# Kernel optimization log

Measured on AMD Instinct MI355X. Metric: run time of the kernel, lower is better.

## Reference

```python
import jax, jax.numpy as jnp
import numpy as np

N, E, P = 50000, 800000, 100000
IN, HID, H, L = 128, 128, 8, 3
D = HID // H


def setup_inputs() -> dict:
    key = jax.random.key(0)
    ks = jax.random.split(key, 24)
    rn = lambda k, shape, s: (jax.random.normal(k, shape, jnp.float32) * s)
    inp = {
        'x': jax.random.normal(ks[0], (N, IN), jnp.float32),
        'edge_src': jax.random.randint(ks[1], (E,), 0, N, jnp.int32),
        'edge_dst': jax.random.randint(ks[2], (E,), 0, N, jnp.int32),
        'edge_w': jax.random.uniform(ks[3], (E,), jnp.float32),
        'pos_src': jax.random.randint(ks[4], (P,), 0, N, jnp.int32),
        'pos_dst': jax.random.randint(ks[5], (P,), 0, N, jnp.int32),
        'neg_src': jax.random.randint(ks[6], (P,), 0, N, jnp.int32),
        'neg_dst': jax.random.randint(ks[7], (P,), 0, N, jnp.int32),
        # input projection
        'W_in': rn(ks[8], (IN, HID), IN ** -0.5),
        'b_in': jnp.zeros((HID,), jnp.float32),
        # per-layer HGT params (single ntype/etype -> plain matrices)
        'Wk': rn(ks[9], (L, HID, HID), HID ** -0.5),
        'Wq': rn(ks[10], (L, HID, HID), HID ** -0.5),
        'Wv': rn(ks[11], (L, HID, HID), HID ** -0.5),
        'att_w': rn(ks[12], (L, H, D, D), D ** -0.5),
        'msg_w': rn(ks[13], (L, H, D, D), D ** -0.5),
        'pri': jnp.ones((L, H), jnp.float32),
        'Wa': rn(ks[14], (L, HID, HID), HID ** -0.5),
        'skip': jnp.ones((L,), jnp.float32),
        # predictor MLP
        'W1': rn(ks[15], (HID, HID // 2), HID ** -0.5),
        'b1': jnp.zeros((HID // 2,), jnp.float32),
        'W2': rn(ks[16], (HID // 2, HID // 4), (HID // 2) ** -0.5),
        'b2': jnp.zeros((HID // 4,), jnp.float32),
        'W3': rn(ks[17], (HID // 4, 1), (HID // 4) ** -0.5),
        'b3': jnp.zeros((1,), jnp.float32),
    }
    return inp


def _hgt_forward(x, edge_src, edge_dst, edge_w, pos_src, pos_dst, neg_src, neg_dst,
                 W_in, b_in, Wk, Wq, Wv, att_w, msg_w, pri, Wa, skip,
                 W1, b1, W2, b2, W3, b3):
    n = x.shape[0]
    nheads = att_w.shape[1]
    d = att_w.shape[2]
    sqrt_d = jnp.asarray(d ** 0.5, x.dtype)
    h = jax.nn.relu(x @ W_in + b_in)
    nlayers = Wk.shape[0]
    for l in range(nlayers):
        k = (h @ Wk[l]).reshape(n, nheads, d)
        q = (h @ Wq[l]).reshape(n, nheads, d)
        v = (h @ Wv[l]).reshape(n, nheads, d)
        # relation-specific per-head transforms (etype constant -> node-level)
        kw = jnp.einsum('nhd,hde->nhe', k, att_w[l])
        mv = jnp.einsum('nhd,hde->nhe', v, msg_w[l])
        # per-edge attention logits [E, H]
        a = (kw[edge_src] * q[edge_dst]).sum(-1) * pri[l] / sqrt_d
        # edge softmax grouped by destination node
        amax = jax.ops.segment_max(a, edge_dst, num_segments=n)[edge_dst]
        ex = jnp.exp(a - amax)
        denom = jax.ops.segment_sum(ex, edge_dst, num_segments=n)[edge_dst]
        attn = ex / denom
        # weighted messages + scatter-sum  [E,H,D] -> [N,H,D]
        m = mv[edge_src] * edge_w[:, None, None] * attn[:, :, None]
        agg = jax.ops.segment_sum(m, edge_dst, num_segments=n).reshape(n, nheads * d)
        hn = agg @ Wa[l]  # linear_a (dropout is identity in eval)
        alpha = jax.nn.sigmoid(skip[l])
        h = hn * alpha + h * (1.0 - alpha)
        if l != nlayers - 1:
            h = jax.nn.relu(h)  # inter-layer relu (dropout identity)
    def predictor(z):
        z = jax.nn.leaky_relu(z @ W1 + b1, 0.2)
        z = jax.nn.leaky_relu(z @ W2 + b2, 0.2)
        return z @ W3 + b3
    h_pos = predictor(h[pos_src] * h[pos_dst])
    h_neg = predictor(h[neg_src] * h[neg_dst])
    return h_pos, h_neg, h


def reference(x, edge_src, edge_dst, edge_w, pos_src, pos_dst, neg_src, neg_dst,
              W_in, b_in, Wk, Wq, Wv, att_w, msg_w, pri, Wa, skip,
              W1, b1, W2, b2, W3, b3):
    return _hgt_forward(x, edge_src, edge_dst, edge_w, pos_src, pos_dst,
                        neg_src, neg_dst, W_in, b_in, Wk, Wq, Wv, att_w,
                        msg_w, pri, Wa, skip, W1, b1, W2, b2, W3, b3)
```

## Files before the change

kernel.cpp:

```cpp
#include <hip/hip_runtime.h>
#include <cstddef>

#define N_NODES 50000
#define N_EDGES 800000
#define N_PAIRS 100000

typedef float floatx4 __attribute__((ext_vector_type(4)));
typedef _Float16 half2v __attribute__((ext_vector_type(2)));
typedef _Float16 half4v __attribute__((ext_vector_type(4)));
typedef _Float16 half8v __attribute__((ext_vector_type(8)));

__device__ inline size_t packA(int m, int k, int K) {
  return ((size_t)((m >> 4) * (K >> 5) + (k >> 5)) << 9) +
         ((((unsigned)k >> 3) & 3) << 7) + ((m & 15) << 3) + (k & 7);
}

__device__ inline float fold_val(int l, int r, int j, const float* Wk, const float* Wq,
                                 const float* Wv, const float* att, const float* msg,
                                 const float* pri) {
  if (j >= 128 && j < 256) return Wq[(l * 128 + r) * 128 + (j - 128)];
  int jj = j & 127, hh = jj >> 4, e = jj & 15;
  const float* W = (j < 128) ? Wk : Wv;
  const float* T = (j < 128) ? att : msg;
  float s = 0.f;
#pragma unroll
  for (int d = 0; d < 16; d++)
    s += W[(l * 128 + r) * 128 + hh * 16 + d] * T[((l * 8 + hh) * 16 + d) * 16 + e];
  if (j < 128) s *= pri[l * 8 + hh] * 0.25f;
  return s;
}

__global__ void wprep_kernel(const float* __restrict__ W_in, const float* __restrict__ Wk,
                             const float* __restrict__ Wq, const float* __restrict__ Wv,
                             const float* __restrict__ att, const float* __restrict__ msg,
                             const float* __restrict__ pri, const float* __restrict__ Wa,
                             const float* __restrict__ W1, const float* __restrict__ W2,
                             _Float16* Wint, _Float16* Wcat, _Float16* Waf,
                             _Float16* W1f, _Float16* W2f) {
  int gid = blockIdx.x * 256 + threadIdx.x;
  float v;
  _Float16* dt;
  size_t o;
  if (gid < 16384) {
    int n = gid >> 7, k = gid & 127;
    v = W_in[k * 128 + n];
    dt = Wint; o = packA(n, k, 128);
  } else if (gid < 163840) {
    int t = gid - 16384;
    int l = t / 49152, u = t - l * 49152;
    int n = u >> 7, k = u & 127;
    v = fold_val(l, k, n, Wk, Wq, Wv, att, msg, pri);
    dt = Wcat + (size_t)l * 49152;
    o = packA(n, k, 128);
  } else if (gid < 212992) {
    int t = gid - 163840;
    int l = t / 16384, u = t & 16383;
    int n = u >> 7, k = u & 127;
    v = Wa[(size_t)l * 16384 + k * 128 + n];
    dt = Waf + (size_t)l * 16384;
    o = packA(n, k, 128);
  } else if (gid < 221184) {
    int u = gid - 212992;
    int n = u >> 7, k = u & 127;
    v = W1[k * 64 + n];
    dt = W1f; o = packA(n, k, 128);
  } else if (gid < 225280) {
    int u = gid - 221184;
    int n = u >> 6, k = u & 63;
    v = (n < 32) ? W2[k * 32 + n] : 0.f;
    dt = W2f; o = packA(n, k, 64);
  } else {
    return;
  }
  dt[o] = (_Float16)v;
}

__global__ void hist_kernel(const int* __restrict__ dst, int* __restrict__ deg, int E) {
  int g = blockIdx.x * blockDim.x + threadIdx.x;
  if (g < E) atomicAdd(&deg[dst[g]], 1);
}

__global__ void scanA_kernel(const int* __restrict__ deg, int* __restrict__ offs,
                             int* __restrict__ bsum, int n) {
  __shared__ int sm[256];
  int t = threadIdx.x;
  int i = blockIdx.x * 256 + t;
  int v = (i < n) ? ((deg[i] + 15) & ~15) : 0;
  sm[t] = v;
  __syncthreads();
  for (int off = 1; off < 256; off <<= 1) {
    int u = (t >= off) ? sm[t - off] : 0;
    __syncthreads();
    sm[t] += u;
    __syncthreads();
  }
  if (i < n) offs[i] = sm[t] - v;
  if (t == 255) bsum[blockIdx.x] = sm[255];
}

__global__ void scanB_kernel(const int* __restrict__ bsum, int* __restrict__ boff,
                             int* __restrict__ offs, int nb, int n) {
  __shared__ int sm[256];
  int t = threadIdx.x;
  int v = (t < nb) ? bsum[t] : 0;
  sm[t] = v;
  __syncthreads();
  for (int off = 1; off < 256; off <<= 1) {
    int u = (t >= off) ? sm[t - off] : 0;
    __syncthreads();
    sm[t] += u;
    __syncthreads();
  }
  boff[t] = sm[t] - v;
  if (t == nb - 1) offs[n] = sm[t];
}

__global__ void scanC_kernel(int* __restrict__ offs, const int* __restrict__ boff,
                             int* __restrict__ cursor, int n) {
  int i = blockIdx.x * 256 + threadIdx.x;
  if (i < n) {
    int o = offs[i] + boff[blockIdx.x];
    offs[i] = o;
    cursor[i] = o;
  }
}

__global__ void scatter_kernel(const int* __restrict__ src, const int* __restrict__ dst,
                               const float* __restrict__ w, int* __restrict__ cursor,
                               int2* __restrict__ eld, int E) {
  int g = blockIdx.x * blockDim.x + threadIdx.x;
  if (g < E) {
    int d = dst[g];
    int p = atomicAdd(&cursor[d], 1);
    eld[p] = make_int2(src[g], __float_as_int(w[g]));
  }
}

__global__ void bhist_kernel(const int* __restrict__ deg, int* __restrict__ bh, int n) {
  __shared__ int lh[256];
  int t = threadIdx.x;
  lh[t] = 0;
  __syncthreads();
  int i = blockIdx.x * 256 + t;
  if (i < n) atomicAdd(&lh[min(deg[i], 255)], 1);
  __syncthreads();
  if (lh[t]) atomicAdd(&bh[t], lh[t]);
}
__global__ void bscan_kernel(const int* __restrict__ bh, int* __restrict__ bcur) {
  __shared__ int sm[256];
  int t = threadIdx.x;
  int v = bh[255 - t];
  sm[t] = v;
  __syncthreads();
  for (int off = 1; off < 256; off <<= 1) {
    int u = (t >= off) ? sm[t - off] : 0;
    __syncthreads();
    sm[t] += u;
    __syncthreads();
  }
  bcur[255 - t] = sm[t] - v;
}
__global__ void bscatter_kernel(const int* __restrict__ deg, int* __restrict__ bcur,
                                int* __restrict__ perm, int n) {
  __shared__ int lh[256], lbase[256];
  int t = threadIdx.x;
  lh[t] = 0;
  __syncthreads();
  int i = blockIdx.x * 256 + t;
  int b = 0, local = 0;
  if (i < n) {
    b = min(deg[i], 255);
    local = atomicAdd(&lh[b], 1);
  }
  __syncthreads();
  int cnt = lh[t];
  lbase[t] = cnt ? atomicAdd(&bcur[t], cnt) : 0;
  __syncthreads();
  if (i < n) perm[lbase[b] + local] = i;
}

template <int FIRST>
__global__ __launch_bounds__(256) void fused_layer(
    const float* __restrict__ x, const _Float16* __restrict__ aggp,
    const _Float16* __restrict__ Wg1, const float* __restrict__ bias,
    const float* __restrict__ skipv, _Float16* __restrict__ hbuf,
    const _Float16* __restrict__ Wcat_l,
    _Float16* __restrict__ kwmv, _Float16* __restrict__ qbuf, int M) {
  int tid = threadIdx.x;
  int wave = tid >> 6, lane = tid & 63;
  int l16 = lane & 15, q = lane >> 4;
  int g = q, mloc = l16;
  int tile = blockIdx.x * 4 + wave;
  int m0 = tile * 16;
  bool alive = m0 < M;
  int tileC = alive ? tile : 0;

  __shared__ _Float16 htile_s[4][2048];
  __shared__ float ldsT_s[4][16 * 68];
  _Float16* htile = htile_s[wave];
  float* myT = ldsT_s[wave];

  half8v a[4];
#pragma unroll
  for (int kc = 0; kc < 4; kc++) {
    if (FIRST) {
      int row = min(m0 + l16, M - 1);
      const float* p = x + (size_t)row * 128 + kc * 32 + q * 8;
      float4 u0 = *(const float4*)p, u1 = *(const float4*)(p + 4);
      float f[8] = {u0.x, u0.y, u0.z, u0.w, u1.x, u1.y, u1.z, u1.w};
      half8v hv;
#pragma unroll
      for (int i = 0; i < 8; i++) hv[i] = (_Float16)f[i];
      a[kc] = hv;
    } else {
      a[kc] = *(const half8v*)(aggp + (size_t)tileC * 2048 + (kc << 9) + lane * 8);
    }
  }

  float alpha = 1.f, beta = 0.f;
  if (!FIRST) {
    float sv = *skipv;
    alpha = 1.f / (1.f + __expf(-sv));
    beta = 1.f - alpha;
  }

  floatx4 acc1[8];
#pragma unroll
  for (int nt = 0; nt < 8; nt++) acc1[nt] = (floatx4){0.f, 0.f, 0.f, 0.f};
#pragma unroll
  for (int kc = 0; kc < 4; kc++) {
    half8v b[8];
#pragma unroll
    for (int nt = 0; nt < 8; nt++)
      b[nt] = *(const half8v*)(Wg1 + (size_t)nt * 2048 + (kc << 9) + lane * 8);
#pragma unroll
    for (int nt = 0; nt < 8; nt++)
      acc1[nt] = __builtin_amdgcn_mfma_f32_16x16x32_f16(a[kc], b[nt], acc1[nt], 0, 0, 0);
  }

#pragma unroll
  for (int p = 0; p < 2; p++) {
    __syncthreads();
#pragma unroll
    for (int ntl = 0; ntl < 4; ntl++)
#pragma unroll
      for (int r = 0; r < 4; r++)
        myT[(q * 4 + r) * 68 + ntl * 16 + l16] = acc1[p * 4 + ntl][r];
    __syncthreads();
#pragma unroll
    for (int kc2 = 0; kc2 < 2; kc2++) {
      const float* rp = myT + mloc * 68 + kc2 * 32 + g * 8;
      floatx4 v0 = *(const floatx4*)rp;
      floatx4 v1 = *(const floatx4*)(rp + 4);
      float vals[8] = {v0[0], v0[1], v0[2], v0[3], v1[0], v1[1], v1[2], v1[3]};
      int col0 = p * 64 + kc2 * 32 + g * 8;
      size_t pbaseL = ((size_t)(tileC * 4 + (col0 >> 5)) << 9) + (size_t)lane * 8;
      if (FIRST) {
        float4 bb0 = *(const float4*)&bias[col0];
        float4 bb1 = *(const float4*)&bias[col0 + 4];
        float bbv[8] = {bb0.x, bb0.y, bb0.z, bb0.w, bb1.x, bb1.y, bb1.z, bb1.w};
#pragma unroll
        for (int j = 0; j < 8; j++) vals[j] = fmaxf(vals[j] + bbv[j], 0.f);
      } else {
        half8v hv = *(const half8v*)(hbuf + pbaseL);
#pragma unroll
        for (int j = 0; j < 8; j++)
          vals[j] = fmaxf(alpha * vals[j] + beta * (float)hv[j], 0.f);
      }
      half8v h8;
#pragma unroll
      for (int j = 0; j < 8; j++) h8[j] = (_Float16)vals[j];
      *(half8v*)(htile + (((p * 2 + kc2) << 9) + (g << 7) + (mloc << 3))) = h8;
      if (alive) *(half8v*)(hbuf + pbaseL) = h8;
    }
  }

  for (int c = 0; c < 6; c++) {
    floatx4 acc2[4];
#pragma unroll
    for (int nt = 0; nt < 4; nt++) acc2[nt] = (floatx4){0.f, 0.f, 0.f, 0.f};
#pragma unroll
    for (int kc = 0; kc < 4; kc++) {
      half8v af = *(const half8v*)(htile + ((kc << 9) + lane * 8));
      half8v b[4];
#pragma unroll
      for (int nt = 0; nt < 4; nt++)
        b[nt] = *(const half8v*)(Wcat_l + (size_t)(c * 4 + nt) * 2048 + (kc << 9) + lane * 8);
#pragma unroll
      for (int nt = 0; nt < 4; nt++)
        acc2[nt] = __builtin_amdgcn_mfma_f32_16x16x32_f16(af, b[nt], acc2[nt], 0, 0, 0);
    }
    __syncthreads();
#pragma unroll
    for (int ntl = 0; ntl < 4; ntl++)
#pragma unroll
      for (int r = 0; r < 4; r++)
        myT[(q * 4 + r) * 68 + ntl * 16 + l16] = acc2[ntl][r];
    __syncthreads();
    if (alive) {
      int row = m0 + mloc;
#pragma unroll
      for (int kc2 = 0; kc2 < 2; kc2++) {
        const float* rp = myT + mloc * 68 + kc2 * 32 + g * 8;
        floatx4 v0 = *(const floatx4*)rp;
        floatx4 v1 = *(const floatx4*)(rp + 4);
        int col0 = c * 64 + kc2 * 32 + g * 8;
        int region = col0 >> 7;
        if (region == 1) {
          half8v h8;
#pragma unroll
          for (int j = 0; j < 4; j++) {
            h8[j] = (_Float16)v0[j];
            h8[j + 4] = (_Float16)v1[j];
          }
          *(half8v*)&qbuf[(size_t)row * 128 + (col0 - 128)] = h8;
        } else {
          int cc = col0 & 127;
          size_t base = (size_t)row * 256 + (size_t)(cc >> 2) * 8 + (region == 2 ? 4 : 0);
          half4v h0, h1;
#pragma unroll
          for (int j = 0; j < 4; j++) {
            h0[j] = (_Float16)v0[j];
            h1[j] = (_Float16)v1[j];
          }
          *(half4v*)&kwmv[base] = h0;
          *(half4v*)&kwmv[base + 8] = h1;
        }
      }
    }
  }
}

__global__ __launch_bounds__(256) void gemm_last(
    const _Float16* __restrict__ aggp, const _Float16* __restrict__ Wg1,
    const float* __restrict__ skipv, const _Float16* __restrict__ hbuf,
    float* __restrict__ hfinal, _Float16* __restrict__ hrow, int M) {
  int tid = threadIdx.x;
  int wave = tid >> 6, lane = tid & 63;
  int l16 = lane & 15, q = lane >> 4;
  int g = q, mloc = l16;
  int tile = blockIdx.x * 4 + wave;
  int m0 = tile * 16;
  bool alive = m0 < M;
  int tileC = alive ? tile : 0;

  __shared__ float ldsT_s[4][16 * 68];
  float* myT = ldsT_s[wave];

  half8v a[4];
#pragma unroll
  for (int kc = 0; kc < 4; kc++)
    a[kc] = *(const half8v*)(aggp + (size_t)tileC * 2048 + (kc << 9) + lane * 8);

  float sv = *skipv;
  float alpha = 1.f / (1.f + __expf(-sv));
  float beta = 1.f - alpha;

  floatx4 acc1[8];
#pragma unroll
  for (int nt = 0; nt < 8; nt++) acc1[nt] = (floatx4){0.f, 0.f, 0.f, 0.f};
#pragma unroll
  for (int kc = 0; kc < 4; kc++) {
    half8v b[8];
#pragma unroll
    for (int nt = 0; nt < 8; nt++)
      b[nt] = *(const half8v*)(Wg1 + (size_t)nt * 2048 + (kc << 9) + lane * 8);
#pragma unroll
    for (int nt = 0; nt < 8; nt++)
      acc1[nt] = __builtin_amdgcn_mfma_f32_16x16x32_f16(a[kc], b[nt], acc1[nt], 0, 0, 0);
  }

#pragma unroll
  for (int p = 0; p < 2; p++) {
    __syncthreads();
#pragma unroll
    for (int ntl = 0; ntl < 4; ntl++)
#pragma unroll
      for (int r = 0; r < 4; r++)
        myT[(q * 4 + r) * 68 + ntl * 16 + l16] = acc1[p * 4 + ntl][r];
    __syncthreads();
    if (alive) {
      int row = m0 + mloc;
#pragma unroll
      for (int kc2 = 0; kc2 < 2; kc2++) {
        const float* rp = myT + mloc * 68 + kc2 * 32 + g * 8;
        floatx4 v0 = *(const floatx4*)rp;
        floatx4 v1 = *(const floatx4*)(rp + 4);
        float vals[8] = {v0[0], v0[1], v0[2], v0[3], v1[0], v1[1], v1[2], v1[3]};
        int col0 = p * 64 + kc2 * 32 + g * 8;
        size_t pbase = ((size_t)(tile * 4 + (col0 >> 5)) << 9) + (size_t)lane * 8;
        half8v hv = *(const half8v*)(hbuf + pbase);
#pragma unroll
        for (int j = 0; j < 8; j++) vals[j] = alpha * vals[j] + beta * (float)hv[j];
        *(float4*)&hfinal[(size_t)row * 128 + col0] =
            make_float4(vals[0], vals[1], vals[2], vals[3]);
        *(float4*)&hfinal[(size_t)row * 128 + col0 + 4] =
            make_float4(vals[4], vals[5], vals[6], vals[7]);
        half8v h8;
#pragma unroll
        for (int j = 0; j < 8; j++) h8[j] = (_Float16)vals[j];
        *(half8v*)&hrow[(size_t)row * 128 + col0] = h8;
      }
    }
  }
}

__global__ __launch_bounds__(256) void pred_fused(
    const _Float16* __restrict__ hrow,
    const int* __restrict__ ps, const int* __restrict__ pd,
    const int* __restrict__ ns, const int* __restrict__ nd,
    const _Float16* __restrict__ W1f, const float* __restrict__ b1,
    const _Float16* __restrict__ W2f, const float* __restrict__ b2,
    const float* __restrict__ W3, const float* __restrict__ b3,
    float* __restrict__ outd, int M) {
  int tid = threadIdx.x;
  int wave = tid >> 6, lane = tid & 63;
  int l16 = lane & 15, q = lane >> 4;
  int g = q, mloc = l16;
  int tile = blockIdx.x * 4 + wave;
  int m0 = tile * 16;
  bool alive = m0 < M;

  __shared__ _Float16 t1_s[4][1024];
  __shared__ float ldsT_s[4][16 * 68];
  _Float16* t1tile = t1_s[wave];
  float* myT = ldsT_s[wave];

  int gr = min(m0 + l16, M - 1);
  bool pos = gr < N_PAIRS;
  int idx = pos ? gr : gr - N_PAIRS;
  int pa = pos ? ps[idx] : ns[idx];
  int pb = pos ? pd[idx] : nd[idx];

  half8v a[4];
#pragma unroll
  for (int kc = 0; kc < 4; kc++) {
    int kbase = kc * 32 + q * 8;
    half8v ha = *(const half8v*)(hrow + (size_t)pa * 128 + kbase);
    half8v hb = *(const half8v*)(hrow + (size_t)pb * 128 + kbase);
    a[kc] = ha * hb;
  }

  floatx4 acc1[4];
#pragma unroll
  for (int nt = 0; nt < 4; nt++) acc1[nt] = (floatx4){0.f, 0.f, 0.f, 0.f};
#pragma unroll
  for (int kc = 0; kc < 4; kc++) {
    half8v b[4];
#pragma unroll
    for (int nt = 0; nt < 4; nt++)
      b[nt] = *(const half8v*)(W1f + (size_t)nt * 2048 + (kc << 9) + lane * 8);
#pragma unroll
    for (int nt = 0; nt < 4; nt++)
      acc1[nt] = __builtin_amdgcn_mfma_f32_16x16x32_f16(a[kc], b[nt], acc1[nt], 0, 0, 0);
  }

  __syncthreads();
#pragma unroll
  for (int ntl = 0; ntl < 4; ntl++)
#pragma unroll
    for (int r = 0; r < 4; r++)
      myT[(q * 4 + r) * 68 + ntl * 16 + l16] = acc1[ntl][r];
  __syncthreads();
#pragma unroll
  for (int kc2 = 0; kc2 < 2; kc2++) {
    const float* rp = myT + mloc * 68 + kc2 * 32 + g * 8;
    floatx4 v0 = *(const floatx4*)rp;
    floatx4 v1 = *(const floatx4*)(rp + 4);
    float vals[8] = {v0[0], v0[1], v0[2], v0[3], v1[0], v1[1], v1[2], v1[3]};
    int col0 = kc2 * 32 + g * 8;
    float4 bb0 = *(const float4*)&b1[col0];
    float4 bb1 = *(const float4*)&b1[col0 + 4];
    float bbv[8] = {bb0.x, bb0.y, bb0.z, bb0.w, bb1.x, bb1.y, bb1.z, bb1.w};
    half8v h8;
#pragma unroll
    for (int j = 0; j < 8; j++) {
      float v = vals[j] + bbv[j];
      v = v > 0.f ? v : 0.2f * v;
      h8[j] = (_Float16)v;
    }
    *(half8v*)(t1tile + ((kc2 << 9) + (g << 7) + (mloc << 3))) = h8;
  }

  floatx4 acc2[2];
#pragma unroll
  for (int nt = 0; nt < 2; nt++) acc2[nt] = (floatx4){0.f, 0.f, 0.f, 0.f};
#pragma unroll
  for (int kc = 0; kc < 2; kc++) {
    half8v af = *(const half8v*)(t1tile + ((kc << 9) + lane * 8));
    half8v b[2];
#pragma unroll
    for (int nt = 0; nt < 2; nt++)
      b[nt] = *(const half8v*)(W2f + (size_t)nt * 1024 + (kc << 9) + lane * 8);
#pragma unroll
    for (int nt = 0; nt < 2; nt++)
      acc2[nt] = __builtin_amdgcn_mfma_f32_16x16x32_f16(af, b[nt], acc2[nt], 0, 0, 0);
  }

  float bw[2], wv[2];
#pragma unroll
  for (int nt = 0; nt < 2; nt++) {
    int col = nt * 16 + l16;
    bw[nt] = b2[col];
    wv[nt] = W3[col];
  }
  float b3v = b3[0];
#pragma unroll
  for (int r = 0; r < 4; r++) {
    float partial = 0.f;
#pragma unroll
    for (int nt = 0; nt < 2; nt++) {
      float v = acc2[nt][r] + bw[nt];
      v = v > 0.f ? v : 0.2f * v;
      partial += v * wv[nt];
    }
    partial += __shfl_xor(partial, 1);
    partial += __shfl_xor(partial, 2);
    partial += __shfl_xor(partial, 4);
    partial += __shfl_xor(partial, 8);
    int row = m0 + q * 4 + r;
    if (l16 == 0 && alive && row < M) outd[row] = partial + b3v;
  }
}

__global__ __launch_bounds__(256) void edge_agg_kernel(
    const _Float16* __restrict__ kwmv, const _Float16* __restrict__ qbuf,
    const int* __restrict__ poffs, const int2* __restrict__ eld,
    const int* __restrict__ perm,
    _Float16* __restrict__ agg, int n) {
  int wslot = blockIdx.x * 4 + (threadIdx.x >> 6);
  int lane = threadIdx.x & 63;
  int hh = lane >> 5;
  int c4 = lane & 31;
  int ch = c4 << 2;
  for (int gw = wslot; gw < n; gw += 8192) {
    int node = perm[gw];
    half4v qv = *(const half4v*)&qbuf[(size_t)node * 128 + ch];
    half2v q01 = {qv[0], qv[1]}, q23 = {qv[2], qv[3]};
    float m = -1e30f, s = 0.f;
    float a0 = 0.f, a1 = 0.f, a2 = 0.f, a3 = 0.f;
    int beg = poffs[node], end = poffs[node + 1];
    for (int j = beg; j < end; j += 16) {
      int2 e[8];
      half8v kvmv[8];
#pragma unroll
      for (int i = 0; i < 8; i++) {
        e[i] = eld[j + 2 * i + hh];
        kvmv[i] = *(const half8v*)&kwmv[(size_t)max(e[i].x, 0) * 256 + (size_t)c4 * 8];
      }
      float p[8];
#pragma unroll
      for (int i = 0; i < 8; i++) {
        half2v k01 = {kvmv[i][0], kvmv[i][1]}, k23 = {kvmv[i][2], kvmv[i][3]};
        float d = __builtin_amdgcn_fdot2(
            k01, q01, __builtin_amdgcn_fdot2(k23, q23, 0.f, false), false);
        d += __shfl_xor(d, 1);
        d += __shfl_xor(d, 2);
        p[i] = (e[i].x >= 0) ? d : -1e30f;
      }
      float nm = m;
#pragma unroll
      for (int i = 0; i < 8; i++) nm = fmaxf(nm, p[i]);
      float sc = __expf(m - nm);
      float t[8];
      float ssum = 0.f;
#pragma unroll
      for (int i = 0; i < 8; i++) {
        t[i] = __expf(p[i] - nm);
        ssum += t[i];
      }
      s = s * sc + ssum;
      a0 *= sc; a1 *= sc; a2 *= sc; a3 *= sc;
#pragma unroll
      for (int i = 0; i < 8; i++) {
        float w = (e[i].x >= 0) ? __int_as_float(e[i].y) : 0.f;
        float f = t[i] * w;
        a0 += f * (float)kvmv[i][4];
        a1 += f * (float)kvmv[i][5];
        a2 += f * (float)kvmv[i][6];
        a3 += f * (float)kvmv[i][7];
      }
      m = nm;
    }
    float mo = __shfl_xor(m, 32);
    float so = __shfl_xor(s, 32);
    float c0 = __shfl_xor(a0, 32), c1 = __shfl_xor(a1, 32);
    float c2 = __shfl_xor(a2, 32), c3 = __shfl_xor(a3, 32);
    float M = fmaxf(m, mo);
    float e1 = __expf(m - M), e2 = __expf(mo - M);
    float st = s * e1 + so * e2;
    float v0 = a0 * e1 + c0 * e2, v1 = a1 * e1 + c1 * e2;
    float v2 = a2 * e1 + c2 * e2, v3 = a3 * e1 + c3 * e2;
    float inv = (st > 0.f) ? 1.f / st : 0.f;
    if (hh == 0) {
      half4v out4;
      out4[0] = (_Float16)(v0 * inv);
      out4[1] = (_Float16)(v1 * inv);
      out4[2] = (_Float16)(v2 * inv);
      out4[3] = (_Float16)(v3 * inv);
      *(half4v*)&agg[packA(node, ch, 128)] = out4;
    }
  }
}

extern "C" void kernel_launch(void* const* d_in, const int* in_sizes, int n_in,
                              void* d_out, int out_size, void* d_ws, size_t ws_size,
                              hipStream_t stream) {
  const float* x        = (const float*)d_in[0];
  const int*   edge_src = (const int*)d_in[1];
  const int*   edge_dst = (const int*)d_in[2];
  const float* edge_w   = (const float*)d_in[3];
  const int*   pos_src  = (const int*)d_in[4];
  const int*   pos_dst  = (const int*)d_in[5];
  const int*   neg_src  = (const int*)d_in[6];
  const int*   neg_dst  = (const int*)d_in[7];
  const float* W_in     = (const float*)d_in[8];
  const float* b_in     = (const float*)d_in[9];
  const float* Wk       = (const float*)d_in[10];
  const float* Wq       = (const float*)d_in[11];
  const float* Wv       = (const float*)d_in[12];
  const float* att_w    = (const float*)d_in[13];
  const float* msg_w    = (const float*)d_in[14];
  const float* pri      = (const float*)d_in[15];
  const float* Wa       = (const float*)d_in[16];
  const float* skip     = (const float*)d_in[17];
  const float* W1       = (const float*)d_in[18];
  const float* b1       = (const float*)d_in[19];
  const float* W2       = (const float*)d_in[20];
  const float* b2       = (const float*)d_in[21];
  const float* W3       = (const float*)d_in[22];
  const float* b3       = (const float*)d_in[23];
  float* out = (float*)d_out;

  char* W = (char*)d_ws;
  _Float16*  qbuf   = (_Float16*)(W + 0);
  _Float16*  kwmv   = (_Float16*)(W + 12800000);
  _Float16*  hbuf   = (_Float16*)(W + 38400000);
  _Float16*  agg    = (_Float16*)(W + 51200000);
  _Float16*  Wint   = (_Float16*)(W + 64000000);
  _Float16*  Wcat   = (_Float16*)(W + 64032768);
  _Float16*  Waf    = (_Float16*)(W + 64327680);
  _Float16*  W1f    = (_Float16*)(W + 64425984);
  _Float16*  W2f    = (_Float16*)(W + 64442368);
  int2*      eld    = (int2*)(W + 64450560);
  int*       deg    = (int*)(W + 77250560);
  int*       poffs  = (int*)(W + 77450560);
  int*       cursor = (int*)(W + 77650576);
  int*       perm   = (int*)(W + 77850576);
  int*       bsum   = (int*)(W + 78050576);
  int*       boff   = (int*)(W + 78051600);
  int*       bh     = (int*)(W + 78052624);
  int*       bcur   = (int*)(W + 78053648);
  _Float16*  hrow   = (_Float16*)(W + 78054912);
  float* hfinal = out + 2 * N_PAIRS;

  hipMemsetAsync(deg, 0, N_NODES * sizeof(int), stream);
  hipMemsetAsync(bh, 0, 1024, stream);
  hipMemsetAsync(eld, 0xFF, 12800000, stream);

  wprep_kernel<<<880, 256, 0, stream>>>(W_in, Wk, Wq, Wv, att_w, msg_w, pri, Wa, W1, W2,
                                        Wint, Wcat, Waf, W1f, W2f);
  hist_kernel<<<(N_EDGES + 255) / 256, 256, 0, stream>>>(edge_dst, deg, N_EDGES);
  scanA_kernel<<<196, 256, 0, stream>>>(deg, poffs, bsum, N_NODES);
  scanB_kernel<<<1, 256, 0, stream>>>(bsum, boff, poffs, 196, N_NODES);
  scanC_kernel<<<196, 256, 0, stream>>>(poffs, boff, cursor, N_NODES);
  scatter_kernel<<<(N_EDGES + 255) / 256, 256, 0, stream>>>(
      edge_src, edge_dst, edge_w, cursor, eld, N_EDGES);
  bhist_kernel<<<196, 256, 0, stream>>>(deg, bh, N_NODES);
  bscan_kernel<<<1, 256, 0, stream>>>(bh, bcur);
  bscatter_kernel<<<196, 256, 0, stream>>>(deg, bcur, perm, N_NODES);

  fused_layer<1><<<782, 256, 0, stream>>>(x, nullptr, Wint, b_in, nullptr, hbuf,
                                          Wcat, kwmv, qbuf, N_NODES);
  edge_agg_kernel<<<2048, 256, 0, stream>>>(kwmv, qbuf, poffs, eld, perm, agg, N_NODES);
  fused_layer<0><<<782, 256, 0, stream>>>(nullptr, agg, Waf, nullptr, skip + 0, hbuf,
                                          Wcat + 49152, kwmv, qbuf, N_NODES);
  edge_agg_kernel<<<2048, 256, 0, stream>>>(kwmv, qbuf, poffs, eld, perm, agg, N_NODES);
  fused_layer<0><<<782, 256, 0, stream>>>(nullptr, agg, Waf + 16384, nullptr, skip + 1,
                                          hbuf, Wcat + 98304, kwmv, qbuf, N_NODES);
  edge_agg_kernel<<<2048, 256, 0, stream>>>(kwmv, qbuf, poffs, eld, perm, agg, N_NODES);
  gemm_last<<<782, 256, 0, stream>>>(agg, Waf + 32768, skip + 2, hbuf,
                                     hfinal, hrow, N_NODES);
  pred_fused<<<3125, 256, 0, stream>>>(hrow, pos_src, pos_dst, neg_src, neg_dst,
                                       W1f, b1, W2f, b2, W3, b3, out, 2 * N_PAIRS);
}
```

Before: 555.8 us.

## Assign one half-wave per destination node and pad edge segments to 8

New measurement: 558.9 us. No clear change (+0.6%).

```diff
diff --git a/kernel.cpp b/kernel.cpp
--- a/kernel.cpp
+++ b/kernel.cpp
@@ -85,7 +85,7 @@
   __shared__ int sm[256];
   int t = threadIdx.x;
   int i = blockIdx.x * 256 + t;
-  int v = (i < n) ? ((deg[i] + 15) & ~15) : 0;
+  int v = (i < n) ? ((deg[i] + 7) & ~7) : 0;
   sm[t] = v;
   __syncthreads();
   for (int off = 1; off < 256; off <<= 1) {
@@ -528,24 +528,23 @@
     const int* __restrict__ poffs, const int2* __restrict__ eld,
     const int* __restrict__ perm,
     _Float16* __restrict__ agg, int n) {
-  int wslot = blockIdx.x * 4 + (threadIdx.x >> 6);
-  int lane = threadIdx.x & 63;
-  int hh = lane >> 5;
-  int c4 = lane & 31;
+  int hw = (blockIdx.x * 256 + threadIdx.x) >> 5;
+  int stride = gridDim.x << 3;
+  int c4 = threadIdx.x & 31;
   int ch = c4 << 2;
-  for (int gw = wslot; gw < n; gw += 8192) {
+  for (int gw = hw; gw < n; gw += stride) {
     int node = perm[gw];
     half4v qv = *(const half4v*)&qbuf[(size_t)node * 128 + ch];
     half2v q01 = {qv[0], qv[1]}, q23 = {qv[2], qv[3]};
     float m = -1e30f, s = 0.f;
     float a0 = 0.f, a1 = 0.f, a2 = 0.f, a3 = 0.f;
     int beg = poffs[node], end = poffs[node + 1];
-    for (int j = beg; j < end; j += 16) {
+    for (int j = beg; j < end; j += 8) {
       int2 e[8];
       half8v kvmv[8];
 #pragma unroll
       for (int i = 0; i < 8; i++) {
-        e[i] = eld[j + 2 * i + hh];
+        e[i] = eld[j + i];
         kvmv[i] = *(const half8v*)&kwmv[(size_t)max(e[i].x, 0) * 256 + (size_t)c4 * 8];
       }
       float p[8];
@@ -582,24 +581,13 @@
       }
       m = nm;
     }
-    float mo = __shfl_xor(m, 32);
-    float so = __shfl_xor(s, 32);
-    float c0 = __shfl_xor(a0, 32), c1 = __shfl_xor(a1, 32);
-    float c2 = __shfl_xor(a2, 32), c3 = __shfl_xor(a3, 32);
-    float M = fmaxf(m, mo);
-    float e1 = __expf(m - M), e2 = __expf(mo - M);
-    float st = s * e1 + so * e2;
-    float v0 = a0 * e1 + c0 * e2, v1 = a1 * e1 + c1 * e2;
-    float v2 = a2 * e1 + c2 * e2, v3 = a3 * e1 + c3 * e2;
-    float inv = (st > 0.f) ? 1.f / st : 0.f;
-    if (hh == 0) {
-      half4v out4;
-      out4[0] = (_Float16)(v0 * inv);
-      out4[1] = (_Float16)(v1 * inv);
-      out4[2] = (_Float16)(v2 * inv);
-      out4[3] = (_Float16)(v3 * inv);
-      *(half4v*)&agg[packA(node, ch, 128)] = out4;
-    }
+    float inv = (s > 0.f) ? 1.f / s : 0.f;
+    half4v out4;
+    out4[0] = (_Float16)(a0 * inv);
+    out4[1] = (_Float16)(a1 * inv);
+    out4[2] = (_Float16)(a2 * inv);
+    out4[3] = (_Float16)(a3 * inv);
+    *(half4v*)&agg[packA(node, ch, 128)] = out4;
   }
 }
 
@@ -656,7 +644,7 @@
 
   hipMemsetAsync(deg, 0, N_NODES * sizeof(int), stream);
   hipMemsetAsync(bh, 0, 1024, stream);
-  hipMemsetAsync(eld, 0xFF, 12800000, stream);
+  hipMemsetAsync(eld, 0xFF, 9600000, stream);
 
   wprep_kernel<<<880, 256, 0, stream>>>(W_in, Wk, Wq, Wv, att_w, msg_w, pri, Wa, W1, W2,
                                         Wint, Wcat, Waf, W1f, W2f);
```
